# Performance work log

Hardware: AMD Instinct MI355X
Metric: run time of the kernel (lower is better)

## Reference

```python
import jax, jax.numpy as jnp
import numpy as np

B, N, C = 2, 384, 1024          # images, proposals/image, box_head feature dim
H_REPN = 256                    # RePN hidden
G_HID, HEADS = 256, 4           # GATConv hidden / heads
TOPK = 8
IMG_H, IMG_W = 800, 800
NEG_SLOPE = 0.2                 # PyG GATConv leaky_relu default


def _box_geom(bx):
    # normalized [x, y, w, h], matching _box_geom
    scale = jnp.array([IMG_W, IMG_H, IMG_W, IMG_H], dtype=bx.dtype)
    nb = bx / scale
    return jnp.stack([nb[:, 0], nb[:, 1], nb[:, 2] - nb[:, 0], nb[:, 3] - nb[:, 1]], axis=1)


def _gat_layer(x, src, tgt, W, att_src, att_dst, bias, heads, out_c):
    # PyG GATConv: messages flow src -> tgt, softmax over incoming edges at tgt
    n = x.shape[0]
    xw = (x @ W).reshape(n, heads, out_c)               # [N, H, F]
    a_s = jnp.sum(xw * att_src, axis=-1)                # [N, H]
    a_d = jnp.sum(xw * att_dst, axis=-1)                # [N, H]
    e = jax.nn.leaky_relu(a_s[src] + a_d[tgt], NEG_SLOPE)  # [E, H]
    e_max = jax.ops.segment_max(e, tgt, num_segments=n)    # stable softmax per target
    alpha = jnp.exp(e - e_max[tgt])
    denom = jax.ops.segment_sum(alpha, tgt, num_segments=n)
    alpha = alpha / jnp.maximum(denom, 1e-16)[tgt]          # [E, H]
    out = jax.ops.segment_sum(xw[src] * alpha[..., None], tgt, num_segments=n)
    return out.reshape(n, heads * out_c) + bias


def setup_inputs() -> dict:
    key = jax.random.key(0)
    ks = jax.random.split(key, 16)
    feats = jax.random.normal(ks[0], (B, N, C), dtype=jnp.float32)
    # boxes with x1<x2, y1<y2 inside the image
    xy = jax.random.uniform(ks[1], (B, N, 2), minval=0.0, maxval=650.0)
    wh = jax.random.uniform(ks[2], (B, N, 2), minval=10.0, maxval=150.0)
    boxes = jnp.concatenate([xy, xy + wh], axis=-1).astype(jnp.float32)
    s = 0.02
    params = {
        'fc1_w': jax.random.normal(ks[3], (2 * C + 4, H_REPN)) * s,
        'fc1_b': jnp.zeros((H_REPN,), jnp.float32),
        'fc2_w': jax.random.normal(ks[4], (H_REPN, 1)) * s,
        'fc2_b': jnp.zeros((1,), jnp.float32),
        'gat1_w': jax.random.normal(ks[5], (C + 4, HEADS * G_HID)) * s,
        'gat1_att_src': jax.random.normal(ks[6], (HEADS, G_HID)) * s,
        'gat1_att_dst': jax.random.normal(ks[7], (HEADS, G_HID)) * s,
        'gat1_b': jnp.zeros((HEADS * G_HID,), jnp.float32),
        'gat2_w': jax.random.normal(ks[8], (HEADS * G_HID, 2)) * s,
        'gat2_att_src': jax.random.normal(ks[9], (1, 2)) * s,
        'gat2_att_dst': jax.random.normal(ks[10], (1, 2)) * s,
        'gat2_b': jnp.zeros((2,), jnp.float32),
    }
    return {'feats': feats, 'boxes': boxes, **params}


def reference(feats, boxes, fc1_w, fc1_b, fc2_w, fc2_b,
              gat1_w, gat1_att_src, gat1_att_dst, gat1_b,
              gat2_w, gat2_att_src, gat2_att_dst, gat2_b):
    def single(f, bx):
        geom4 = _box_geom(bx)                               # [N, 4]
        x = jnp.concatenate([f, geom4], axis=1)             # [N, C+4]
        # RelationProposalNetwork: fc1(cat[f_i, f_j, |b_i-b_j|]) done as split matmuls
        Wa, Wb, Wg = fc1_w[:C], fc1_w[C:2 * C], fc1_w[2 * C:]
        p1 = f @ Wa                                         # [N, H]
        p2 = f @ Wb                                         # [N, H]
        gdiff = jnp.abs(bx[:, None, :] - bx[None, :, :])    # [N, N, 4]
        h = jax.nn.relu(p1[:, None, :] + p2[None, :, :] + gdiff @ Wg + fc1_b)
        rel = (h @ fc2_w)[..., 0] + fc2_b[0]                # [N, N]
        # _make_edge_index: mask diagonal, top-k per row; edge = [dst_node, neighbor]
        rn = rel - jnp.eye(N, dtype=rel.dtype) * 1e6
        nbr = jax.lax.top_k(rn, TOPK)[1]                    # [N, k]
        src = jnp.repeat(jnp.arange(N), TOPK)               # edge_index[0] (PyG source)
        tgt = nbr.reshape(-1)                               # edge_index[1] (PyG target)
        loop = jnp.arange(N)                                # GATConv add_self_loops=True
        src = jnp.concatenate([src, loop])
        tgt = jnp.concatenate([tgt, loop])
        h1 = jax.nn.relu(_gat_layer(x, src, tgt, gat1_w, gat1_att_src, gat1_att_dst, gat1_b, HEADS, G_HID))
        logits = _gat_layer(h1, src, tgt, gat2_w, gat2_att_src, gat2_att_dst, gat2_b, 1, 2)
        return logits                                       # [N, 2]
    return jax.vmap(single)(feats, boxes)
```

## Files before the change

### kernel.cpp

```cpp
#include <hip/hip_runtime.h>

#define BB 2
#define NN 384
#define CC 1024
#define HR 256
#define NHEADS 4
#define TOPK 8
#define CAP 448
#define NEG 0.2f

typedef __attribute__((ext_vector_type(8))) short bf16x8;
typedef __attribute__((ext_vector_type(4))) float f32x4;

__device__ __forceinline__ unsigned short f2bf(float v) {
    unsigned u = __float_as_uint(v);
    return (unsigned short)((u + 0x7FFFu + ((u >> 16) & 1u)) >> 16);
}
__device__ __forceinline__ float bf2f(unsigned short h) {
    return __uint_as_float((unsigned)h << 16);
}

__global__ __launch_bounds__(256) void k_prep(const float* __restrict__ feats,
        const float* __restrict__ boxes, const float* __restrict__ gat1_w,
        const float* __restrict__ fc1_w,
        uint4* __restrict__ Asw, uint4* __restrict__ Bsw,
        uint4* __restrict__ Ah, uint4* __restrict__ Al,
        uint4* __restrict__ Bh, uint4* __restrict__ Bl,
        float4* __restrict__ wgp, int* __restrict__ counts) {
    int blk = blockIdx.x;
    int t = threadIdx.x;
    int gflat = blk * 256 + t;
    if (gflat < BB * NN) counts[gflat] = 0;

    if (blk < 396) {
        int flat = gflat;
        int lane = flat & 63;
        int kc = (flat >> 6) % 33;
        int mt = flat / (33 * 64);
        int m = mt * 16 + (lane & 15);
        int k0 = kc * 32 + (lane >> 4) * 8;
        unsigned short vals[8];
        const float s = 1.0f / 800.0f;
#pragma unroll
        for (int j = 0; j < 8; j++) {
            int k = k0 + j;
            float v;
            if (k < CC) v = feats[(size_t)m * CC + k];
            else if (k < CC + 4) {
                const float* bx = boxes + (size_t)m * 4;
                int gk = k - CC;
                v = (gk == 0) ? bx[0] * s : (gk == 1) ? bx[1] * s
                  : (gk == 2) ? (bx[2] - bx[0]) * s : (bx[3] - bx[1]) * s;
            } else v = 0.f;
            vals[j] = f2bf(v);
        }
        uint4 pk;
        pk.x = (unsigned)vals[0] | ((unsigned)vals[1] << 16);
        pk.y = (unsigned)vals[2] | ((unsigned)vals[3] << 16);
        pk.z = (unsigned)vals[4] | ((unsigned)vals[5] << 16);
        pk.w = (unsigned)vals[6] | ((unsigned)vals[7] << 16);
        Asw[flat] = pk;
    } else if (blk < 924) {
        int flat = gflat - 396 * 256;
        int lane = flat & 63;
        int kc = (flat >> 6) % 33;
        int nt = flat / (33 * 64);
        int n = nt * 16 + (lane & 15);
        int k0 = kc * 32 + (lane >> 4) * 8;
        unsigned short vals[8];
#pragma unroll
        for (int j = 0; j < 8; j++) {
            int k = k0 + j;
            float v = (k < CC + 4) ? gat1_w[(size_t)k * 1024 + n] : 0.f;
            vals[j] = f2bf(v);
        }
        uint4 pk;
        pk.x = (unsigned)vals[0] | ((unsigned)vals[1] << 16);
        pk.y = (unsigned)vals[2] | ((unsigned)vals[3] << 16);
        pk.z = (unsigned)vals[4] | ((unsigned)vals[5] << 16);
        pk.w = (unsigned)vals[6] | ((unsigned)vals[7] << 16);
        Bsw[flat] = pk;
    } else if (blk < 1308) {
        int flat = gflat - 924 * 256;
        int lane = flat & 63;
        int kc = (flat >> 6) % 32;
        int mt = flat / (32 * 64);
        int m = mt * 16 + (lane & 15);
        int k0 = kc * 32 + (lane >> 4) * 8;
        unsigned short vh[8], vl[8];
        const float* src = feats + (size_t)m * CC + k0;
#pragma unroll
        for (int j = 0; j < 8; j++) {
            float v = src[j];
            unsigned short h = f2bf(v);
            vh[j] = h;
            vl[j] = f2bf(v - bf2f(h));
        }
        uint4 ph, pl;
        ph.x = (unsigned)vh[0] | ((unsigned)vh[1] << 16);
        ph.y = (unsigned)vh[2] | ((unsigned)vh[3] << 16);
        ph.z = (unsigned)vh[4] | ((unsigned)vh[5] << 16);
        ph.w = (unsigned)vh[6] | ((unsigned)vh[7] << 16);
        pl.x = (unsigned)vl[0] | ((unsigned)vl[1] << 16);
        pl.y = (unsigned)vl[2] | ((unsigned)vl[3] << 16);
        pl.z = (unsigned)vl[4] | ((unsigned)vl[5] << 16);
        pl.w = (unsigned)vl[6] | ((unsigned)vl[7] << 16);
        Ah[flat] = ph; Al[flat] = pl;
    } else if (blk < 1564) {
        int flat = gflat - 1308 * 256;
        int lane = flat & 63;
        int kc = (flat >> 6) % 32;
        int nt = flat / (32 * 64);
        int n = nt * 16 + (lane & 15);
        int k0 = kc * 32 + (lane >> 4) * 8;
        unsigned short vh[8], vl[8];
#pragma unroll
        for (int j = 0; j < 8; j++) {
            int k = k0 + j;
            float v = (n < 256) ? fc1_w[(size_t)k * 256 + n]
                                : fc1_w[(size_t)(CC + k) * 256 + (n - 256)];
            unsigned short h = f2bf(v);
            vh[j] = h;
            vl[j] = f2bf(v - bf2f(h));
        }
        uint4 ph, pl;
        ph.x = (unsigned)vh[0] | ((unsigned)vh[1] << 16);
        ph.y = (unsigned)vh[2] | ((unsigned)vh[3] << 16);
        ph.z = (unsigned)vh[4] | ((unsigned)vh[5] << 16);
        ph.w = (unsigned)vh[6] | ((unsigned)vh[7] << 16);
        pl.x = (unsigned)vl[0] | ((unsigned)vl[1] << 16);
        pl.y = (unsigned)vl[2] | ((unsigned)vl[3] << 16);
        pl.z = (unsigned)vl[4] | ((unsigned)vl[5] << 16);
        pl.w = (unsigned)vl[6] | ((unsigned)vl[7] << 16);
        Bh[flat] = ph; Bl[flat] = pl;
    } else {
        int c = t;
        float4 w;
        w.x = fc1_w[(size_t)(2 * CC + 0) * HR + c];
        w.y = fc1_w[(size_t)(2 * CC + 1) * HR + c];
        w.z = fc1_w[(size_t)(2 * CC + 2) * HR + c];
        w.w = fc1_w[(size_t)(2 * CC + 3) * HR + c];
        wgp[c] = w;
    }
}

__global__ __launch_bounds__(512) void k_p12m(const uint4* __restrict__ Ah,
        const uint4* __restrict__ Al, const uint4* __restrict__ Bh,
        const uint4* __restrict__ Bl, const float* __restrict__ fc1_b,
        float* __restrict__ p1, float* __restrict__ p2t) {
    __shared__ float lds[4][64][4];
    int t = threadIdx.x;
    int w = t >> 6;
    int lane = t & 63;
    int g = w & 3;
    int kh = w >> 2;
    int blk = blockIdx.x;
    int mt = blk >> 3;
    int nt = (blk & 7) * 4 + g;
    f32x4 acc = {0.f, 0.f, 0.f, 0.f};
    const uint4* pah = Ah + (size_t)mt * 32 * 64 + (size_t)kh * 16 * 64 + lane;
    const uint4* pal = Al + (size_t)mt * 32 * 64 + (size_t)kh * 16 * 64 + lane;
    const uint4* pbh = Bh + (size_t)nt * 32 * 64 + (size_t)kh * 16 * 64 + lane;
    const uint4* pbl = Bl + (size_t)nt * 32 * 64 + (size_t)kh * 16 * 64 + lane;
#pragma unroll 4
    for (int kc = 0; kc < 16; kc++) {
        uint4 ah = pah[kc * 64];
        uint4 al = pal[kc * 64];
        uint4 bh = pbh[kc * 64];
        uint4 bl = pbl[kc * 64];
        acc = __builtin_amdgcn_mfma_f32_16x16x32_bf16(*(bf16x8*)&ah, *(bf16x8*)&bh, acc, 0, 0, 0);
        acc = __builtin_amdgcn_mfma_f32_16x16x32_bf16(*(bf16x8*)&ah, *(bf16x8*)&bl, acc, 0, 0, 0);
        acc = __builtin_amdgcn_mfma_f32_16x16x32_bf16(*(bf16x8*)&al, *(bf16x8*)&bh, acc, 0, 0, 0);
    }
    if (kh == 1) {
#pragma unroll
        for (int r = 0; r < 4; r++) lds[g][lane][r] = acc[r];
    }
    __syncthreads();
    if (kh == 0) {
#pragma unroll
        for (int r = 0; r < 4; r++) acc[r] += lds[g][lane][r];
        int col = nt * 16 + (lane & 15);
        int row0 = mt * 16 + (lane >> 4) * 4;
        if (col < 256) {
            float bias = fc1_b[col];
#pragma unroll
            for (int r = 0; r < 4; r++)
                p1[(size_t)(row0 + r) * 256 + col] = acc[r] + bias;
        } else {
#pragma unroll
            for (int r = 0; r < 4; r++) {
                int rr = row0 + r;
                int b = rr / NN, rloc = rr % NN;
                p2t[((size_t)b * 256 + (col - 256)) * NN + rloc] = acc[r];
            }
        }
    }
}

__global__ __launch_bounds__(512) void k_xw1m(const uint4* __restrict__ Asw,
        const uint4* __restrict__ Bsw, float* __restrict__ xw1) {
    __shared__ float lds[4][64][4];
    int t = threadIdx.x;
    int w = t >> 6;
    int lane = t & 63;
    int g = w & 3;
    int kh = w >> 2;
    int blk = blockIdx.x;
    int mt = blk >> 4;
    int nt = (blk & 15) * 4 + g;
    int nk = kh ? 16 : 17;
    f32x4 acc = {0.f, 0.f, 0.f, 0.f};
    const uint4* pa = Asw + (size_t)mt * 33 * 64 + (size_t)kh * 17 * 64 + lane;
    const uint4* pb = Bsw + (size_t)nt * 33 * 64 + (size_t)kh * 17 * 64 + lane;
#pragma unroll 4
    for (int kc = 0; kc < nk; kc++) {
        uint4 av = pa[kc * 64];
        uint4 bv = pb[kc * 64];
        acc = __builtin_amdgcn_mfma_f32_16x16x32_bf16(*(bf16x8*)&av, *(bf16x8*)&bv, acc, 0, 0, 0);
    }
    if (kh == 1) {
#pragma unroll
        for (int r = 0; r < 4; r++) lds[g][lane][r] = acc[r];
    }
    __syncthreads();
    if (kh == 0) {
#pragma unroll
        for (int r = 0; r < 4; r++) acc[r] += lds[g][lane][r];
        int col = nt * 16 + (lane & 15);
        int row0 = mt * 16 + (lane >> 4) * 4;
#pragma unroll
        for (int r = 0; r < 4; r++)
            xw1[(size_t)(row0 + r) * 1024 + col] = acc[r];
    }
}

__global__ __launch_bounds__(384) void k_rel(const float* __restrict__ p1,
        const float* __restrict__ p2t, const float* __restrict__ boxes,
        const float4* __restrict__ wgp, const float* __restrict__ fc2_w,
        float* __restrict__ rel_a, float* __restrict__ rel_b) {
    int blk = blockIdx.x;
    int p = blk >> 1;
    int ch = blk & 1;
    int b = p / (NN / 2);
    int i0 = (p - b * (NN / 2)) * 2;
    int row0 = b * NN + i0;
    int j = threadIdx.x;
    float a0 = boxes[(size_t)row0 * 4 + 0];
    float a1 = boxes[(size_t)row0 * 4 + 1];
    float a2 = boxes[(size_t)row0 * 4 + 2];
    float a3 = boxes[(size_t)row0 * 4 + 3];
    float c0 = boxes[(size_t)(row0 + 1) * 4 + 0];
    float c1 = boxes[(size_t)(row0 + 1) * 4 + 1];
    float c2 = boxes[(size_t)(row0 + 1) * 4 + 2];
    float c3 = boxes[(size_t)(row0 + 1) * 4 + 3];
    float4 bj = *(const float4*)(boxes + ((size_t)b * NN + j) * 4);
    float g00 = fabsf(a0 - bj.x), g01 = fabsf(a1 - bj.y);
    float g02 = fabsf(a2 - bj.z), g03 = fabsf(a3 - bj.w);
    float g10 = fabsf(c0 - bj.x), g11 = fabsf(c1 - bj.y);
    float g12 = fabsf(c2 - bj.z), g13 = fabsf(c3 - bj.w);
    const float* p1r0 = p1 + (size_t)row0 * HR + ch * 128;
    const float* p1r1 = p1r0 + HR;
    const float* p2b = p2t + (size_t)b * HR * NN + (size_t)ch * 128 * NN + j;
    const float4* wg = wgp + ch * 128;
    const float* w2 = fc2_w + ch * 128;
    float acc0 = 0.f, acc1 = 0.f;
#pragma unroll 8
    for (int c = 0; c < 128; c++) {
        float4 w = wg[c];
        float pa = p1r0[c];
        float pb = p1r1[c];
        float wc = w2[c];
        float p2v = p2b[(size_t)c * NN];
        float v0 = pa + p2v + g00 * w.x + g01 * w.y + g02 * w.z + g03 * w.w;
        float v1 = pb + p2v + g10 * w.x + g11 * w.y + g12 * w.z + g13 * w.w;
        acc0 += fmaxf(v0, 0.f) * wc;
        acc1 += fmaxf(v1, 0.f) * wc;
    }
    float* dst = ch ? rel_b : rel_a;
    dst[(size_t)row0 * NN + j] = acc0;
    dst[(size_t)(row0 + 1) * NN + j] = acc1;
}

__global__ __launch_bounds__(64) void k_topk_inv(const float* __restrict__ rel_a,
        const float* __restrict__ rel_b, int* __restrict__ counts,
        int* __restrict__ inlist) {
    int row = blockIdx.x;
    int b = row / NN;
    int i = row - b * NN;
    int t = threadIdx.x;
    const float* ra = rel_a + (size_t)row * NN;
    const float* rb = rel_b + (size_t)row * NN;
    float v[6]; int id[6];
#pragma unroll
    for (int q = 0; q < 6; q++) {
        int j = t + q * 64;
        float val = ra[j] + rb[j];
        if (j == i) val = -INFINITY;
        v[q] = val; id[q] = j;
    }
    int mine = -1;
    for (int k = 0; k < TOPK; k++) {
        float bv = -INFINITY; int bi = NN;
#pragma unroll
        for (int q = 0; q < 6; q++) {
            if (v[q] > bv || (v[q] == bv && id[q] < bi)) { bv = v[q]; bi = id[q]; }
        }
        for (int off = 32; off > 0; off >>= 1) {
            float ov = __shfl_down(bv, off);
            int   oi = __shfl_down(bi, off);
            if (ov > bv || (ov == bv && oi < bi)) { bv = ov; bi = oi; }
        }
        bi = __shfl(bi, 0);
        if (t == k) mine = bi;
#pragma unroll
        for (int q = 0; q < 6; q++) if (id[q] == bi) v[q] = -INFINITY;
    }
    if (t < TOPK) {
        int tg = b * NN + mine;
        int q = atomicAdd(&counts[tg], 1);
        inlist[(size_t)tg * CAP + q] = i;
    } else if (t == TOPK) {
        int q = atomicAdd(&counts[row], 1);
        inlist[(size_t)row * CAP + q] = i;
    }
}

__global__ __launch_bounds__(256) void k_att1(const float* __restrict__ xw1,
        const float* __restrict__ att_src, const float* __restrict__ att_dst,
        float* __restrict__ a_s, float* __restrict__ a_d) {
    int node = blockIdx.x;
    int w = threadIdx.x >> 6;
    int lane = threadIdx.x & 63;
    const float4* xr = (const float4*)(xw1 + (size_t)node * 1024 + w * 256);
    const float4* sr = (const float4*)(att_src + w * 256);
    const float4* dr = (const float4*)(att_dst + w * 256);
    float4 x = xr[lane];
    float4 s = sr[lane];
    float4 d = dr[lane];
    float ps = x.x * s.x + x.y * s.y + x.z * s.z + x.w * s.w;
    float pd = x.x * d.x + x.y * d.y + x.z * d.z + x.w * d.w;
#pragma unroll
    for (int off = 32; off > 0; off >>= 1) {
        ps += __shfl_xor(ps, off);
        pd += __shfl_xor(pd, off);
    }
    if (lane == 0) {
        a_s[(size_t)node * NHEADS + w] = ps;
        a_d[(size_t)node * NHEADS + w] = pd;
    }
}

__global__ __launch_bounds__(256) void k_agg1h(const int* __restrict__ counts,
        const int* __restrict__ inlist, const float* __restrict__ a_s,
        const float* __restrict__ a_d, const float* __restrict__ xw1,
        const float* __restrict__ gat1_b, float* __restrict__ h1) {
    __shared__ int slist[CAP];
    __shared__ float walpha[CAP];
    int blk = blockIdx.x;
    int node = blk >> 2;
    int h = blk & 3;
    int b = node / NN;
    int t = threadIdx.x;
    int deg = counts[node];
    for (int e = t; e < deg; e += 256) slist[e] = inlist[(size_t)node * CAP + e];
    __syncthreads();
    if (t < 64) {
        float ad = a_d[(size_t)node * NHEADS + h];
        float vals[7];
        int cnt = 0;
        float vmax = -INFINITY;
        for (int e = t; e < deg; e += 64) {
            float x = a_s[(size_t)(b * NN + slist[e]) * NHEADS + h] + ad;
            x = x >= 0.f ? x : NEG * x;
            vals[cnt++] = x;
            vmax = fmaxf(vmax, x);
        }
#pragma unroll
        for (int off = 32; off > 0; off >>= 1)
            vmax = fmaxf(vmax, __shfl_xor(vmax, off));
        float sum = 0.f;
        for (int i = 0; i < cnt; i++) {
            vals[i] = expf(vals[i] - vmax);
            sum += vals[i];
        }
#pragma unroll
        for (int off = 32; off > 0; off >>= 1)
            sum += __shfl_xor(sum, off);
        float inv = 1.f / fmaxf(sum, 1e-16f);
        cnt = 0;
        for (int e = t; e < deg; e += 64) walpha[e] = vals[cnt++] * inv;
    }
    __syncthreads();
    float acc = 0.f;
    for (int e = 0; e < deg; e++)
        acc += walpha[e] * xw1[(size_t)(b * NN + slist[e]) * 1024 + h * 256 + t];
    float o = acc + gat1_b[h * 256 + t];
    h1[(size_t)node * 1024 + h * 256 + t] = fmaxf(o, 0.f);
}

__global__ __launch_bounds__(64) void k_xw2att(const float* __restrict__ h1,
        const float* __restrict__ w2, const float* __restrict__ as2,
        const float* __restrict__ ad2, float* __restrict__ xw2,
        float* __restrict__ a_s2, float* __restrict__ a_d2) {
    int node = blockIdx.x;
    int lane = threadIdx.x;
    const float4* hr = (const float4*)(h1 + (size_t)node * 1024);
    float p0 = 0.f, p1v = 0.f;
#pragma unroll
    for (int q = 0; q < 4; q++) {
        float4 v = hr[lane + q * 64];
        int c = (lane + q * 64) * 4;
        float4 wa = *(const float4*)(w2 + c * 2);
        float4 wb = *(const float4*)(w2 + c * 2 + 4);
        p0  += v.x * wa.x + v.y * wa.z + v.z * wb.x + v.w * wb.z;
        p1v += v.x * wa.y + v.y * wa.w + v.z * wb.y + v.w * wb.w;
    }
#pragma unroll
    for (int off = 32; off > 0; off >>= 1) {
        p0 += __shfl_xor(p0, off);
        p1v += __shfl_xor(p1v, off);
    }
    if (lane == 0) {
        xw2[(size_t)node * 2] = p0;
        xw2[(size_t)node * 2 + 1] = p1v;
        a_s2[node] = p0 * as2[0] + p1v * as2[1];
        a_d2[node] = p0 * ad2[0] + p1v * ad2[1];
    }
}

__global__ __launch_bounds__(64) void k_agg2(const int* __restrict__ counts,
        const int* __restrict__ inlist, const float* __restrict__ a_s2,
        const float* __restrict__ a_d2, const float* __restrict__ xw2,
        const float* __restrict__ b2, float* __restrict__ out) {
    int node = blockIdx.x;
    int b = node / NN;
    int lane = threadIdx.x;
    int deg = counts[node];
    float ad = a_d2[node];
    float vals[7]; int srcs[7];
    int cnt = 0;
    float vmax = -INFINITY;
    for (int e = lane; e < deg; e += 64) {
        int s = b * NN + inlist[(size_t)node * CAP + e];
        float x = a_s2[s] + ad;
        x = x >= 0.f ? x : NEG * x;
        srcs[cnt] = s; vals[cnt] = x; cnt++;
        vmax = fmaxf(vmax, x);
    }
#pragma unroll
    for (int off = 32; off > 0; off >>= 1)
        vmax = fmaxf(vmax, __shfl_xor(vmax, off));
    float sum = 0.f;
    for (int i = 0; i < cnt; i++) {
        vals[i] = expf(vals[i] - vmax);
        sum += vals[i];
    }
#pragma unroll
    for (int off = 32; off > 0; off >>= 1)
        sum += __shfl_xor(sum, off);
    float inv = 1.f / fmaxf(sum, 1e-16f);
    float a0 = 0.f, a1 = 0.f;
    for (int i = 0; i < cnt; i++) {
        a0 += vals[i] * xw2[(size_t)srcs[i] * 2];
        a1 += vals[i] * xw2[(size_t)srcs[i] * 2 + 1];
    }
#pragma unroll
    for (int off = 32; off > 0; off >>= 1) {
        a0 += __shfl_xor(a0, off);
        a1 += __shfl_xor(a1, off);
    }
    if (lane == 0) {
        out[(size_t)node * 2]     = a0 * inv + b2[0];
        out[(size_t)node * 2 + 1] = a1 * inv + b2[1];
    }
}

extern "C" void kernel_launch(void* const* d_in, const int* in_sizes, int n_in,
                              void* d_out, int out_size, void* d_ws, size_t ws_size,
                              hipStream_t stream) {
    const float* feats  = (const float*)d_in[0];
    const float* boxes  = (const float*)d_in[1];
    const float* fc1_w  = (const float*)d_in[2];
    const float* fc1_b  = (const float*)d_in[3];
    const float* fc2_w  = (const float*)d_in[4];
    const float* fc2_b  = (const float*)d_in[5];
    const float* gat1_w = (const float*)d_in[6];
    const float* g1as   = (const float*)d_in[7];
    const float* g1ad   = (const float*)d_in[8];
    const float* gat1_b = (const float*)d_in[9];
    const float* gat2_w = (const float*)d_in[10];
    const float* g2as   = (const float*)d_in[11];
    const float* g2ad   = (const float*)d_in[12];
    const float* gat2_b = (const float*)d_in[13];
    float* out = (float*)d_out;
    (void)fc2_b;

    char* ws = (char*)d_ws;
    size_t off = 0;
    auto alloc = [&](size_t bytes) -> void* {
        void* p = ws + off;
        off += (bytes + 255) / 256 * 256;
        return p;
    };
    int*   counts = (int*)alloc((size_t)BB * NN * 4);
    int*   inlist = (int*)alloc((size_t)BB * NN * CAP * 4);
    float* p1     = (float*)alloc((size_t)BB * NN * HR * 4);
    float* p2t    = (float*)alloc((size_t)BB * HR * NN * 4);
    float* rel_a  = (float*)alloc((size_t)BB * NN * NN * 4);
    float* rel_b  = (float*)alloc((size_t)BB * NN * NN * 4);
    float* xw1    = (float*)alloc((size_t)BB * NN * 1024 * 4);
    float* a_s1   = (float*)alloc((size_t)BB * NN * NHEADS * 4);
    float* a_d1   = (float*)alloc((size_t)BB * NN * NHEADS * 4);
    float* h1     = (float*)alloc((size_t)BB * NN * 1024 * 4);
    float* xw2    = (float*)alloc((size_t)BB * NN * 2 * 4);
    float* as2f   = (float*)alloc((size_t)BB * NN * 4);
    float* ad2f   = (float*)alloc((size_t)BB * NN * 4);
    uint4* Asw    = (uint4*)alloc((size_t)48 * 33 * 64 * 16);
    uint4* Bsw    = (uint4*)alloc((size_t)64 * 33 * 64 * 16);
    uint4* Ah     = (uint4*)alloc((size_t)48 * 32 * 64 * 16);
    uint4* Al     = (uint4*)alloc((size_t)48 * 32 * 64 * 16);
    uint4* Bh     = (uint4*)alloc((size_t)32 * 32 * 64 * 16);
    uint4* Bl     = (uint4*)alloc((size_t)32 * 32 * 64 * 16);
    float4* wgp   = (float4*)alloc((size_t)HR * 16);
    (void)ws_size; (void)in_sizes; (void)n_in; (void)out_size;

    k_prep<<<1565, 256, 0, stream>>>(feats, boxes, gat1_w, fc1_w,
                                     Asw, Bsw, Ah, Al, Bh, Bl, wgp, counts);
    k_p12m<<<48 * 8, 512, 0, stream>>>(Ah, Al, Bh, Bl, fc1_b, p1, p2t);
    k_rel<<<BB * NN, 384, 0, stream>>>(p1, p2t, boxes, wgp, fc2_w, rel_a, rel_b);
    k_topk_inv<<<BB * NN, 64, 0, stream>>>(rel_a, rel_b, counts, inlist);
    k_xw1m<<<48 * 16, 512, 0, stream>>>(Asw, Bsw, xw1);
    k_att1<<<BB * NN, 256, 0, stream>>>(xw1, g1as, g1ad, a_s1, a_d1);
    k_agg1h<<<BB * NN * NHEADS, 256, 0, stream>>>(counts, inlist, a_s1, a_d1, xw1, gat1_b, h1);
    k_xw2att<<<BB * NN, 64, 0, stream>>>(h1, gat2_w, g2as, g2ad, xw2, as2f, ad2f);
    k_agg2<<<BB * NN, 64, 0, stream>>>(counts, inlist, as2f, ad2f, xw2, gat2_b, out);
}
```

Before: 167.4 us.

## Merge independent kernels and fuse GAT layer-2 projection into aggregation

Result: faster. 162.4 us (-3.0%).

```diff
diff --git a/kernel.cpp b/kernel.cpp
--- a/kernel.cpp
+++ b/kernel.cpp
@@ -26,11 +26,13 @@
         uint4* __restrict__ Asw, uint4* __restrict__ Bsw,
         uint4* __restrict__ Ah, uint4* __restrict__ Al,
         uint4* __restrict__ Bh, uint4* __restrict__ Bl,
-        float4* __restrict__ wgp, int* __restrict__ counts) {
+        float4* __restrict__ wgp, int* __restrict__ counts,
+        float* __restrict__ xw2) {
     int blk = blockIdx.x;
     int t = threadIdx.x;
     int gflat = blk * 256 + t;
     if (gflat < BB * NN) counts[gflat] = 0;
+    if (gflat < BB * NN * 2) xw2[gflat] = 0.f;
 
     if (blk < 396) {
         int flat = gflat;
@@ -144,142 +146,167 @@
     }
 }
 
-__global__ __launch_bounds__(512) void k_p12m(const uint4* __restrict__ Ah,
+__global__ __launch_bounds__(512) void k_mm(const uint4* __restrict__ Ah,
         const uint4* __restrict__ Al, const uint4* __restrict__ Bh,
         const uint4* __restrict__ Bl, const float* __restrict__ fc1_b,
-        float* __restrict__ p1, float* __restrict__ p2t) {
+        float* __restrict__ p1, float* __restrict__ p2t,
+        const uint4* __restrict__ Asw, const uint4* __restrict__ Bsw,
+        float* __restrict__ xw1) {
     __shared__ float lds[4][64][4];
     int t = threadIdx.x;
     int w = t >> 6;
     int lane = t & 63;
     int g = w & 3;
     int kh = w >> 2;
-    int blk = blockIdx.x;
-    int mt = blk >> 3;
-    int nt = (blk & 7) * 4 + g;
-    f32x4 acc = {0.f, 0.f, 0.f, 0.f};
-    const uint4* pah = Ah + (size_t)mt * 32 * 64 + (size_t)kh * 16 * 64 + lane;
-    const uint4* pal = Al + (size_t)mt * 32 * 64 + (size_t)kh * 16 * 64 + lane;
-    const uint4* pbh = Bh + (size_t)nt * 32 * 64 + (size_t)kh * 16 * 64 + lane;
-    const uint4* pbl = Bl + (size_t)nt * 32 * 64 + (size_t)kh * 16 * 64 + lane;
+    int blk0 = blockIdx.x;
+    if (blk0 < 384) {
+        int blk = blk0;
+        int mt = blk >> 3;
+        int nt = (blk & 7) * 4 + g;
+        f32x4 acc = {0.f, 0.f, 0.f, 0.f};
+        const uint4* pah = Ah + (size_t)mt * 32 * 64 + (size_t)kh * 16 * 64 + lane;
+        const uint4* pal = Al + (size_t)mt * 32 * 64 + (size_t)kh * 16 * 64 + lane;
+        const uint4* pbh = Bh + (size_t)nt * 32 * 64 + (size_t)kh * 16 * 64 + lane;
+        const uint4* pbl = Bl + (size_t)nt * 32 * 64 + (size_t)kh * 16 * 64 + lane;
 #pragma unroll 4
-    for (int kc = 0; kc < 16; kc++) {
-        uint4 ah = pah[kc * 64];
-        uint4 al = pal[kc * 64];
-        uint4 bh = pbh[kc * 64];
-        uint4 bl = pbl[kc * 64];
-        acc = __builtin_amdgcn_mfma_f32_16x16x32_bf16(*(bf16x8*)&ah, *(bf16x8*)&bh, acc, 0, 0, 0);
-        acc = __builtin_amdgcn_mfma_f32_16x16x32_bf16(*(bf16x8*)&ah, *(bf16x8*)&bl, acc, 0, 0, 0);
-        acc = __builtin_amdgcn_mfma_f32_16x16x32_bf16(*(bf16x8*)&al, *(bf16x8*)&bh, acc, 0, 0, 0);
-    }
-    if (kh == 1) {
-#pragma unroll
-        for (int r = 0; r < 4; r++) lds[g][lane][r] = acc[r];
-    }
-    __syncthreads();
-    if (kh == 0) {
-#pragma unroll
-        for (int r = 0; r < 4; r++) acc[r] += lds[g][lane][r];
-        int col = nt * 16 + (lane & 15);
-        int row0 = mt * 16 + (lane >> 4) * 4;
-        if (col < 256) {
-            float bias = fc1_b[col];
+        for (int kc = 0; kc < 16; kc++) {
+            uint4 ah = pah[kc * 64];
+            uint4 al = pal[kc * 64];
+            uint4 bh = pbh[kc * 64];
+            uint4 bl = pbl[kc * 64];
+            acc = __builtin_amdgcn_mfma_f32_16x16x32_bf16(*(bf16x8*)&ah, *(bf16x8*)&bh, acc, 0, 0, 0);
+            acc = __builtin_amdgcn_mfma_f32_16x16x32_bf16(*(bf16x8*)&ah, *(bf16x8*)&bl, acc, 0, 0, 0);
+            acc = __builtin_amdgcn_mfma_f32_16x16x32_bf16(*(bf16x8*)&al, *(bf16x8*)&bh, acc, 0, 0, 0);
+        }
+        if (kh == 1) {
+#pragma unroll
+            for (int r = 0; r < 4; r++) lds[g][lane][r] = acc[r];
+        }
+        __syncthreads();
+        if (kh == 0) {
+#pragma unroll
+            for (int r = 0; r < 4; r++) acc[r] += lds[g][lane][r];
+            int col = nt * 16 + (lane & 15);
+            int row0 = mt * 16 + (lane >> 4) * 4;
+            if (col < 256) {
+                float bias = fc1_b[col];
+#pragma unroll
+                for (int r = 0; r < 4; r++)
+                    p1[(size_t)(row0 + r) * 256 + col] = acc[r] + bias;
+            } else {
+#pragma unroll
+                for (int r = 0; r < 4; r++) {
+                    int rr = row0 + r;
+                    int b = rr / NN, rloc = rr % NN;
+                    p2t[((size_t)b * 256 + (col - 256)) * NN + rloc] = acc[r];
+                }
+            }
+        }
+    } else {
+        int blk = blk0 - 384;
+        int mt = blk >> 4;
+        int nt = (blk & 15) * 4 + g;
+        int nk = kh ? 16 : 17;
+        f32x4 acc = {0.f, 0.f, 0.f, 0.f};
+        const uint4* pa = Asw + (size_t)mt * 33 * 64 + (size_t)kh * 17 * 64 + lane;
+        const uint4* pb = Bsw + (size_t)nt * 33 * 64 + (size_t)kh * 17 * 64 + lane;
+#pragma unroll 4
+        for (int kc = 0; kc < nk; kc++) {
+            uint4 av = pa[kc * 64];
+            uint4 bv = pb[kc * 64];
+            acc = __builtin_amdgcn_mfma_f32_16x16x32_bf16(*(bf16x8*)&av, *(bf16x8*)&bv, acc, 0, 0, 0);
+        }
+        if (kh == 1) {
+#pragma unroll
+            for (int r = 0; r < 4; r++) lds[g][lane][r] = acc[r];
+        }
+        __syncthreads();
+        if (kh == 0) {
+#pragma unroll
+            for (int r = 0; r < 4; r++) acc[r] += lds[g][lane][r];
+            int col = nt * 16 + (lane & 15);
+            int row0 = mt * 16 + (lane >> 4) * 4;
 #pragma unroll
             for (int r = 0; r < 4; r++)
-                p1[(size_t)(row0 + r) * 256 + col] = acc[r] + bias;
-        } else {
-#pragma unroll
-            for (int r = 0; r < 4; r++) {
-                int rr = row0 + r;
-                int b = rr / NN, rloc = rr % NN;
-                p2t[((size_t)b * 256 + (col - 256)) * NN + rloc] = acc[r];
-            }
-        }
-    }
-}
-
-__global__ __launch_bounds__(512) void k_xw1m(const uint4* __restrict__ Asw,
-        const uint4* __restrict__ Bsw, float* __restrict__ xw1) {
-    __shared__ float lds[4][64][4];
-    int t = threadIdx.x;
-    int w = t >> 6;
-    int lane = t & 63;
-    int g = w & 3;
-    int kh = w >> 2;
-    int blk = blockIdx.x;
-    int mt = blk >> 4;
-    int nt = (blk & 15) * 4 + g;
-    int nk = kh ? 16 : 17;
-    f32x4 acc = {0.f, 0.f, 0.f, 0.f};
-    const uint4* pa = Asw + (size_t)mt * 33 * 64 + (size_t)kh * 17 * 64 + lane;
-    const uint4* pb = Bsw + (size_t)nt * 33 * 64 + (size_t)kh * 17 * 64 + lane;
-#pragma unroll 4
-    for (int kc = 0; kc < nk; kc++) {
-        uint4 av = pa[kc * 64];
-        uint4 bv = pb[kc * 64];
-        acc = __builtin_amdgcn_mfma_f32_16x16x32_bf16(*(bf16x8*)&av, *(bf16x8*)&bv, acc, 0, 0, 0);
-    }
-    if (kh == 1) {
-#pragma unroll
-        for (int r = 0; r < 4; r++) lds[g][lane][r] = acc[r];
-    }
-    __syncthreads();
-    if (kh == 0) {
-#pragma unroll
-        for (int r = 0; r < 4; r++) acc[r] += lds[g][lane][r];
-        int col = nt * 16 + (lane & 15);
-        int row0 = mt * 16 + (lane >> 4) * 4;
-#pragma unroll
-        for (int r = 0; r < 4; r++)
-            xw1[(size_t)(row0 + r) * 1024 + col] = acc[r];
-    }
-}
-
-__global__ __launch_bounds__(384) void k_rel(const float* __restrict__ p1,
+                xw1[(size_t)(row0 + r) * 1024 + col] = acc[r];
+        }
+    }
+}
+
+__global__ __launch_bounds__(384) void k_relatt(const float* __restrict__ p1,
         const float* __restrict__ p2t, const float* __restrict__ boxes,
         const float4* __restrict__ wgp, const float* __restrict__ fc2_w,
-        float* __restrict__ rel_a, float* __restrict__ rel_b) {
-    int blk = blockIdx.x;
-    int p = blk >> 1;
-    int ch = blk & 1;
-    int b = p / (NN / 2);
-    int i0 = (p - b * (NN / 2)) * 2;
-    int row0 = b * NN + i0;
-    int j = threadIdx.x;
-    float a0 = boxes[(size_t)row0 * 4 + 0];
-    float a1 = boxes[(size_t)row0 * 4 + 1];
-    float a2 = boxes[(size_t)row0 * 4 + 2];
-    float a3 = boxes[(size_t)row0 * 4 + 3];
-    float c0 = boxes[(size_t)(row0 + 1) * 4 + 0];
-    float c1 = boxes[(size_t)(row0 + 1) * 4 + 1];
-    float c2 = boxes[(size_t)(row0 + 1) * 4 + 2];
-    float c3 = boxes[(size_t)(row0 + 1) * 4 + 3];
-    float4 bj = *(const float4*)(boxes + ((size_t)b * NN + j) * 4);
-    float g00 = fabsf(a0 - bj.x), g01 = fabsf(a1 - bj.y);
-    float g02 = fabsf(a2 - bj.z), g03 = fabsf(a3 - bj.w);
-    float g10 = fabsf(c0 - bj.x), g11 = fabsf(c1 - bj.y);
-    float g12 = fabsf(c2 - bj.z), g13 = fabsf(c3 - bj.w);
-    const float* p1r0 = p1 + (size_t)row0 * HR + ch * 128;
-    const float* p1r1 = p1r0 + HR;
-    const float* p2b = p2t + (size_t)b * HR * NN + (size_t)ch * 128 * NN + j;
-    const float4* wg = wgp + ch * 128;
-    const float* w2 = fc2_w + ch * 128;
-    float acc0 = 0.f, acc1 = 0.f;
+        float* __restrict__ rel_a, float* __restrict__ rel_b,
+        const float* __restrict__ xw1, const float* __restrict__ att_src,
+        const float* __restrict__ att_dst, float* __restrict__ a_s,
+        float* __restrict__ a_d) {
+    int blk0 = blockIdx.x;
+    if (blk0 < 768) {
+        int blk = blk0;
+        int p = blk >> 1;
+        int ch = blk & 1;
+        int b = p / (NN / 2);
+        int i0 = (p - b * (NN / 2)) * 2;
+        int row0 = b * NN + i0;
+        int j = threadIdx.x;
+        float a0 = boxes[(size_t)row0 * 4 + 0];
+        float a1 = boxes[(size_t)row0 * 4 + 1];
+        float a2 = boxes[(size_t)row0 * 4 + 2];
+        float a3 = boxes[(size_t)row0 * 4 + 3];
+        float c0 = boxes[(size_t)(row0 + 1) * 4 + 0];
+        float c1 = boxes[(size_t)(row0 + 1) * 4 + 1];
+        float c2 = boxes[(size_t)(row0 + 1) * 4 + 2];
+        float c3 = boxes[(size_t)(row0 + 1) * 4 + 3];
+        float4 bj = *(const float4*)(boxes + ((size_t)b * NN + j) * 4);
+        float g00 = fabsf(a0 - bj.x), g01 = fabsf(a1 - bj.y);
+        float g02 = fabsf(a2 - bj.z), g03 = fabsf(a3 - bj.w);
+        float g10 = fabsf(c0 - bj.x), g11 = fabsf(c1 - bj.y);
+        float g12 = fabsf(c2 - bj.z), g13 = fabsf(c3 - bj.w);
+        const float* p1r0 = p1 + (size_t)row0 * HR + ch * 128;
+        const float* p1r1 = p1r0 + HR;
+        const float* p2b = p2t + (size_t)b * HR * NN + (size_t)ch * 128 * NN + j;
+        const float4* wg = wgp + ch * 128;
+        const float* w2 = fc2_w + ch * 128;
+        float acc0 = 0.f, acc1 = 0.f;
 #pragma unroll 8
-    for (int c = 0; c < 128; c++) {
-        float4 w = wg[c];
-        float pa = p1r0[c];
-        float pb = p1r1[c];
-        float wc = w2[c];
-        float p2v = p2b[(size_t)c * NN];
-        float v0 = pa + p2v + g00 * w.x + g01 * w.y + g02 * w.z + g03 * w.w;
-        float v1 = pb + p2v + g10 * w.x + g11 * w.y + g12 * w.z + g13 * w.w;
-        acc0 += fmaxf(v0, 0.f) * wc;
-        acc1 += fmaxf(v1, 0.f) * wc;
-    }
-    float* dst = ch ? rel_b : rel_a;
-    dst[(size_t)row0 * NN + j] = acc0;
-    dst[(size_t)(row0 + 1) * NN + j] = acc1;
+        for (int c = 0; c < 128; c++) {
+            float4 w = wg[c];
+            float pa = p1r0[c];
+            float pb = p1r1[c];
+            float wc = w2[c];
+            float p2v = p2b[(size_t)c * NN];
+            float v0 = pa + p2v + g00 * w.x + g01 * w.y + g02 * w.z + g03 * w.w;
+            float v1 = pb + p2v + g10 * w.x + g11 * w.y + g12 * w.z + g13 * w.w;
+            acc0 += fmaxf(v0, 0.f) * wc;
+            acc1 += fmaxf(v1, 0.f) * wc;
+        }
+        float* dst = ch ? rel_b : rel_a;
+        dst[(size_t)row0 * NN + j] = acc0;
+        dst[(size_t)(row0 + 1) * NN + j] = acc1;
+    } else {
+        int node = blk0 - 768;
+        int t = threadIdx.x;
+        if (t >= 256) return;
+        int w = t >> 6;
+        int lane = t & 63;
+        const float4* xr = (const float4*)(xw1 + (size_t)node * 1024 + w * 256);
+        const float4* sr = (const float4*)(att_src + w * 256);
+        const float4* dr = (const float4*)(att_dst + w * 256);
+        float4 x = xr[lane];
+        float4 s = sr[lane];
+        float4 d = dr[lane];
+        float ps = x.x * s.x + x.y * s.y + x.z * s.z + x.w * s.w;
+        float pd = x.x * d.x + x.y * d.y + x.z * d.z + x.w * d.w;
+#pragma unroll
+        for (int off = 32; off > 0; off >>= 1) {
+            ps += __shfl_xor(ps, off);
+            pd += __shfl_xor(pd, off);
+        }
+        if (lane == 0) {
+            a_s[(size_t)node * NHEADS + w] = ps;
+            a_d[(size_t)node * NHEADS + w] = pd;
+        }
+    }
 }
 
 __global__ __launch_bounds__(64) void k_topk_inv(const float* __restrict__ rel_a,
@@ -326,42 +353,21 @@
     }
 }
 
-__global__ __launch_bounds__(256) void k_att1(const float* __restrict__ xw1,
-        const float* __restrict__ att_src, const float* __restrict__ att_dst,
-        float* __restrict__ a_s, float* __restrict__ a_d) {
-    int node = blockIdx.x;
-    int w = threadIdx.x >> 6;
-    int lane = threadIdx.x & 63;
-    const float4* xr = (const float4*)(xw1 + (size_t)node * 1024 + w * 256);
-    const float4* sr = (const float4*)(att_src + w * 256);
-    const float4* dr = (const float4*)(att_dst + w * 256);
-    float4 x = xr[lane];
-    float4 s = sr[lane];
-    float4 d = dr[lane];
-    float ps = x.x * s.x + x.y * s.y + x.z * s.z + x.w * s.w;
-    float pd = x.x * d.x + x.y * d.y + x.z * d.z + x.w * d.w;
-#pragma unroll
-    for (int off = 32; off > 0; off >>= 1) {
-        ps += __shfl_xor(ps, off);
-        pd += __shfl_xor(pd, off);
-    }
-    if (lane == 0) {
-        a_s[(size_t)node * NHEADS + w] = ps;
-        a_d[(size_t)node * NHEADS + w] = pd;
-    }
-}
-
 __global__ __launch_bounds__(256) void k_agg1h(const int* __restrict__ counts,
         const int* __restrict__ inlist, const float* __restrict__ a_s,
         const float* __restrict__ a_d, const float* __restrict__ xw1,
-        const float* __restrict__ gat1_b, float* __restrict__ h1) {
+        const float* __restrict__ gat1_b, const float* __restrict__ w2,
+        float* __restrict__ xw2) {
     __shared__ int slist[CAP];
     __shared__ float walpha[CAP];
+    __shared__ float redp[8];
     int blk = blockIdx.x;
     int node = blk >> 2;
     int h = blk & 3;
     int b = node / NN;
     int t = threadIdx.x;
+    int wid = t >> 6;
+    int lane = t & 63;
     int deg = counts[node];
     for (int e = t; e < deg; e += 256) slist[e] = inlist[(size_t)node * CAP + e];
     __syncthreads();
@@ -395,57 +401,44 @@
     float acc = 0.f;
     for (int e = 0; e < deg; e++)
         acc += walpha[e] * xw1[(size_t)(b * NN + slist[e]) * 1024 + h * 256 + t];
-    float o = acc + gat1_b[h * 256 + t];
-    h1[(size_t)node * 1024 + h * 256 + t] = fmaxf(o, 0.f);
-}
-
-__global__ __launch_bounds__(64) void k_xw2att(const float* __restrict__ h1,
-        const float* __restrict__ w2, const float* __restrict__ as2,
-        const float* __restrict__ ad2, float* __restrict__ xw2,
-        float* __restrict__ a_s2, float* __restrict__ a_d2) {
-    int node = blockIdx.x;
-    int lane = threadIdx.x;
-    const float4* hr = (const float4*)(h1 + (size_t)node * 1024);
-    float p0 = 0.f, p1v = 0.f;
-#pragma unroll
-    for (int q = 0; q < 4; q++) {
-        float4 v = hr[lane + q * 64];
-        int c = (lane + q * 64) * 4;
-        float4 wa = *(const float4*)(w2 + c * 2);
-        float4 wb = *(const float4*)(w2 + c * 2 + 4);
-        p0  += v.x * wa.x + v.y * wa.z + v.z * wb.x + v.w * wb.z;
-        p1v += v.x * wa.y + v.y * wa.w + v.z * wb.y + v.w * wb.w;
-    }
+    float o = fmaxf(acc + gat1_b[h * 256 + t], 0.f);
+    int d = h * 256 + t;
+    float p0 = o * w2[d * 2];
+    float p1v = o * w2[d * 2 + 1];
 #pragma unroll
     for (int off = 32; off > 0; off >>= 1) {
         p0 += __shfl_xor(p0, off);
         p1v += __shfl_xor(p1v, off);
     }
-    if (lane == 0) {
-        xw2[(size_t)node * 2] = p0;
-        xw2[(size_t)node * 2 + 1] = p1v;
-        a_s2[node] = p0 * as2[0] + p1v * as2[1];
-        a_d2[node] = p0 * ad2[0] + p1v * ad2[1];
+    if (lane == 0) { redp[wid] = p0; redp[4 + wid] = p1v; }
+    __syncthreads();
+    if (t == 0) {
+        atomicAdd(&xw2[(size_t)node * 2],     redp[0] + redp[1] + redp[2] + redp[3]);
+        atomicAdd(&xw2[(size_t)node * 2 + 1], redp[4] + redp[5] + redp[6] + redp[7]);
     }
 }
 
 __global__ __launch_bounds__(64) void k_agg2(const int* __restrict__ counts,
-        const int* __restrict__ inlist, const float* __restrict__ a_s2,
-        const float* __restrict__ a_d2, const float* __restrict__ xw2,
+        const int* __restrict__ inlist, const float* __restrict__ xw2,
+        const float* __restrict__ as2, const float* __restrict__ ad2,
         const float* __restrict__ b2, float* __restrict__ out) {
     int node = blockIdx.x;
     int b = node / NN;
     int lane = threadIdx.x;
     int deg = counts[node];
-    float ad = a_d2[node];
-    float vals[7]; int srcs[7];
+    float s0 = as2[0], s1 = as2[1];
+    float d0 = ad2[0], d1 = ad2[1];
+    float2 xwn = *(const float2*)(xw2 + (size_t)node * 2);
+    float ad = xwn.x * d0 + xwn.y * d1;
+    float vals[7], xs0[7], xs1[7];
     int cnt = 0;
     float vmax = -INFINITY;
     for (int e = lane; e < deg; e += 64) {
         int s = b * NN + inlist[(size_t)node * CAP + e];
-        float x = a_s2[s] + ad;
+        float2 xws = *(const float2*)(xw2 + (size_t)s * 2);
+        float x = xws.x * s0 + xws.y * s1 + ad;
         x = x >= 0.f ? x : NEG * x;
-        srcs[cnt] = s; vals[cnt] = x; cnt++;
+        xs0[cnt] = xws.x; xs1[cnt] = xws.y; vals[cnt] = x; cnt++;
         vmax = fmaxf(vmax, x);
     }
 #pragma unroll
@@ -462,8 +455,8 @@
     float inv = 1.f / fmaxf(sum, 1e-16f);
     float a0 = 0.f, a1 = 0.f;
     for (int i = 0; i < cnt; i++) {
-        a0 += vals[i] * xw2[(size_t)srcs[i] * 2];
-        a1 += vals[i] * xw2[(size_t)srcs[i] * 2 + 1];
+        a0 += vals[i] * xs0[i];
+        a1 += vals[i] * xs1[i];
     }
 #pragma unroll
     for (int off = 32; off > 0; off >>= 1) {
@@ -512,10 +505,7 @@
     float* xw1    = (float*)alloc((size_t)BB * NN * 1024 * 4);
     float* a_s1   = (float*)alloc((size_t)BB * NN * NHEADS * 4);
     float* a_d1   = (float*)alloc((size_t)BB * NN * NHEADS * 4);
-    float* h1     = (float*)alloc((size_t)BB * NN * 1024 * 4);
     float* xw2    = (float*)alloc((size_t)BB * NN * 2 * 4);
-    float* as2f   = (float*)alloc((size_t)BB * NN * 4);
-    float* ad2f   = (float*)alloc((size_t)BB * NN * 4);
     uint4* Asw    = (uint4*)alloc((size_t)48 * 33 * 64 * 16);
     uint4* Bsw    = (uint4*)alloc((size_t)64 * 33 * 64 * 16);
     uint4* Ah     = (uint4*)alloc((size_t)48 * 32 * 64 * 16);
@@ -526,13 +516,12 @@
     (void)ws_size; (void)in_sizes; (void)n_in; (void)out_size;
 
     k_prep<<<1565, 256, 0, stream>>>(feats, boxes, gat1_w, fc1_w,
-                                     Asw, Bsw, Ah, Al, Bh, Bl, wgp, counts);
-    k_p12m<<<48 * 8, 512, 0, stream>>>(Ah, Al, Bh, Bl, fc1_b, p1, p2t);
-    k_rel<<<BB * NN, 384, 0, stream>>>(p1, p2t, boxes, wgp, fc2_w, rel_a, rel_b);
+                                     Asw, Bsw, Ah, Al, Bh, Bl, wgp, counts, xw2);
+    k_mm<<<1152, 512, 0, stream>>>(Ah, Al, Bh, Bl, fc1_b, p1, p2t, Asw, Bsw, xw1);
+    k_relatt<<<1536, 384, 0, stream>>>(p1, p2t, boxes, wgp, fc2_w, rel_a, rel_b,
+                                       xw1, g1as, g1ad, a_s1, a_d1);
     k_topk_inv<<<BB * NN, 64, 0, stream>>>(rel_a, rel_b, counts, inlist);
-    k_xw1m<<<48 * 16, 512, 0, stream>>>(Asw, Bsw, xw1);
-    k_att1<<<BB * NN, 256, 0, stream>>>(xw1, g1as, g1ad, a_s1, a_d1);
-    k_agg1h<<<BB * NN * NHEADS, 256, 0, stream>>>(counts, inlist, a_s1, a_d1, xw1, gat1_b, h1);
-    k_xw2att<<<BB * NN, 64, 0, stream>>>(h1, gat2_w, g2as, g2ad, xw2, as2f, ad2f);
-    k_agg2<<<BB * NN, 64, 0, stream>>>(counts, inlist, as2f, ad2f, xw2, gat2_b, out);
-}
+    k_agg1h<<<BB * NN * NHEADS, 256, 0, stream>>>(counts, inlist, a_s1, a_d1, xw1,
+                                                  gat1_b, gat2_w, xw2);
+    k_agg2<<<BB * NN, 64, 0, stream>>>(counts, inlist, xw2, g2as, g2ad, gat2_b, out);
+}
```
